# Kernel optimization log

Hardware: AMD Instinct MI355X
Metric: run time of the kernel (lower is better)

The kernel has to match this reference:

```python
import jax, jax.numpy as jnp
import numpy as np

N = 100000      # num nodes
E = 800000      # num edges
IN = 128        # in_channels
OUT = 128       # out_channels
ALPHA = 0.5


def setup_inputs() -> dict:
    key = jax.random.key(0)
    k1, k2, k3, k4, k5, k6 = jax.random.split(key, 6)
    x = jax.random.normal(k1, (N, IN), dtype=jnp.float32)
    edge_index = jax.random.randint(k2, (2, E), 0, N, dtype=jnp.int32)
    # GCNConv linear weights (glorot-ish) and biases for both directions
    s = 1.0 / np.sqrt(IN)
    W_sd = jax.random.normal(k3, (IN, OUT), dtype=jnp.float32) * s
    b_sd = jnp.zeros((OUT,), dtype=jnp.float32)
    W_ds = jax.random.normal(k4, (IN, OUT), dtype=jnp.float32) * s
    b_ds = jnp.zeros((OUT,), dtype=jnp.float32)
    return {"x": x, "edge_index": edge_index, "W_sd": W_sd, "b_sd": b_sd,
            "W_ds": W_ds, "b_ds": b_ds}


def _dir_gcn_norm_weights(row, col, dtype):
    """edge_weight = out_deg_inv_sqrt[row] * in_deg_inv_sqrt[col] (unit input weights)."""
    ones = jnp.ones((row.shape[0],), dtype=dtype)
    in_deg = jax.ops.segment_sum(ones, col, num_segments=N)
    out_deg = jax.ops.segment_sum(ones, row, num_segments=N)
    in_inv = jnp.where(in_deg > 0, jax.lax.rsqrt(in_deg), 0.0).astype(dtype)
    out_inv = jnp.where(out_deg > 0, jax.lax.rsqrt(out_deg), 0.0).astype(dtype)
    return out_inv[row] * in_inv[col]


def _gcn_conv(x, W, b, src, dst, w):
    """GCNConv(normalize=False, add_self_loops=False): lin -> gather -> scale -> scatter-add -> +bias."""
    h = x @ W                                   # [N, OUT]
    msg = h[src] * w[:, None]                   # [E, OUT]
    return jax.ops.segment_sum(msg, dst, num_segments=N) + b


def reference(x, edge_index, W_sd, b_sd, W_ds, b_ds):
    row, col = edge_index[0], edge_index[1]
    # forward-direction norm (src->dst) and transposed-graph norm (edge_index.flip(0))
    w = _dir_gcn_norm_weights(row, col, x.dtype)
    w_t = _dir_gcn_norm_weights(col, row, x.dtype)
    # conv_dst_to_src uses transposed edges: source=col, dest=row
    x_in = _gcn_conv(x, W_ds, b_ds, col, row, w_t)
    # conv_src_to_dst uses original edges: source=row, dest=col
    x_out = _gcn_conv(x, W_sd, b_sd, row, col, w)
    return ALPHA * x_in + (1.0 - ALPHA) * x_out
```

## Files before the change

kernel.cpp:

```cpp
#include <hip/hip_runtime.h>

#define NN 100000
#define NE 800000
#define NI 1600000
#define NB 391
#define IPB 6250

#define OFF_INV    0u
#define OFF_OFFS   800000u
#define OFF_BB     1600008u
#define OFF_HIST   1601600u
#define OFF_CSRC   2001984u
#define OFF_XB     8401984u
#define OFF_AGG    34001984u
#define OFF_PAIRS  34001984u
#define OFF_WT     85201984u
#define OFF_BIAS   85267520u
#define OFF_TOT    85268032u

typedef short short8 __attribute__((ext_vector_type(8)));
typedef unsigned short u16x8 __attribute__((ext_vector_type(8)));
typedef float f32x4 __attribute__((ext_vector_type(4)));
typedef float f32x8 __attribute__((ext_vector_type(8)));

__device__ __forceinline__ unsigned short f2bf(float f) {
    unsigned u = __float_as_uint(f);
    u = (u + 0x7FFFu + ((u >> 16) & 1u)) >> 16;
    return (unsigned short)u;
}
__device__ __forceinline__ float b2f(unsigned short h) {
    return __uint_as_float(((unsigned)h) << 16);
}
__device__ __forceinline__ f32x8 bvec2f(u16x8 v) {
    f32x8 r;
#pragma unroll
    for (int i = 0; i < 8; ++i) r[i] = b2f(v[i]);
    return r;
}


__global__ __launch_bounds__(256) void k_hist(const int* __restrict__ ei,
                                              int* __restrict__ hist) {
    __shared__ int h[NB];
    for (int k = threadIdx.x; k < NB; k += 256) h[k] = 0;
    __syncthreads();
    int base = blockIdx.x * IPB;
    for (int t = threadIdx.x; t < IPB; t += 256) {
        int i = base + t;
        int key = (i < NE) ? ei[i] : (NN + ei[i]);
        atomicAdd(&h[key >> 9], 1);
    }
    __syncthreads();
    for (int k = threadIdx.x; k < NB; k += 256) hist[k * 256 + blockIdx.x] = h[k];
}

__global__ __launch_bounds__(256) void k_red(const int* __restrict__ hist,
                                             int* __restrict__ tot) {
    __shared__ int s[256];
    int k = blockIdx.x;
    s[threadIdx.x] = hist[k * 256 + threadIdx.x];
    __syncthreads();
    for (int st = 128; st > 0; st >>= 1) {
        if (threadIdx.x < st) s[threadIdx.x] += s[threadIdx.x + st];
        __syncthreads();
    }
    if (threadIdx.x == 0) tot[k] = s[0];
}

__global__ __launch_bounds__(512) void k_scan_tot(const int* __restrict__ tot,
                                                  int* __restrict__ bb) {
    __shared__ int sA[512], sB[512];
    int tid = threadIdx.x;
    int v = (tid < NB) ? tot[tid] : 0;
    sA[tid] = v;
    __syncthreads();
    int *src = sA, *dst = sB;
    for (int st = 1; st < 512; st <<= 1) {
        dst[tid] = src[tid] + ((tid >= st) ? src[tid - st] : 0);
        __syncthreads();
        int* tp = src; src = dst; dst = tp;
    }
    if (tid <= NB) bb[tid] = (tid > 0) ? src[tid - 1] : 0;
}

__global__ __launch_bounds__(256) void k_rebase(int* __restrict__ hist,
                                                const int* __restrict__ bb) {
    __shared__ int sA[256], sB[256];
    int k = blockIdx.x, tid = threadIdx.x;
    int v = hist[k * 256 + tid];
    sA[tid] = v;
    __syncthreads();
    int *src = sA, *dst = sB;
    for (int st = 1; st < 256; st <<= 1) {
        dst[tid] = src[tid] + ((tid >= st) ? src[tid - st] : 0);
        __syncthreads();
        int* tp = src; src = dst; dst = tp;
    }
    hist[k * 256 + tid] = bb[k] + src[tid] - v;
}

__global__ __launch_bounds__(256) void k_scatter(const int* __restrict__ ei,
                                                 const int* __restrict__ hist,
                                                 unsigned long long* __restrict__ pairs) {
    __shared__ int cur[NB];
    for (int k = threadIdx.x; k < NB; k += 256) cur[k] = hist[k * 256 + blockIdx.x];
    __syncthreads();
    int base = blockIdx.x * IPB;
    for (int t = threadIdx.x; t < IPB; t += 256) {
        int i = base + t;
        int e = ei[i];
        int key, val;
        if (i < NE) { key = e;      val = ei[NE + i]; }
        else        { key = NN + e; val = ei[i - NE]; }
        int pos = atomicAdd(&cur[key >> 9], 1);
        pairs[pos] = (((unsigned long long)(unsigned)key) << 32) | (unsigned)val;
    }
}

__global__ __launch_bounds__(256) void k_bucket(const unsigned long long* __restrict__ pairs,
                                                const int* __restrict__ bb,
                                                int* __restrict__ csr_src,
                                                int* __restrict__ offsets,
                                                float* __restrict__ inv) {
    __shared__ int sA[512], sB[512], cur[512];
    const int h = blockIdx.x, tid = threadIdx.x;
    const int s0 = bb[h], s1 = bb[h + 1];
    for (int k = tid; k < 512; k += 256) sA[k] = 0;
    __syncthreads();
    for (int i = s0 + tid; i < s1; i += 256) {
        int key = (int)(pairs[i] >> 32);
        atomicAdd(&sA[key & 511], 1);
    }
    __syncthreads();
    int *src = sA, *dst = sB;
    for (int st = 1; st < 512; st <<= 1) {
        for (int k = tid; k < 512; k += 256) dst[k] = src[k] + ((k >= st) ? src[k - st] : 0);
        __syncthreads();
        int* tp = src; src = dst; dst = tp;
    }
    for (int k = tid; k < 512; k += 256) {
        int incl = src[k];
        int excl = (k > 0) ? src[k - 1] : 0;
        cur[k] = s0 + excl;
        int gkey = h * 512 + k;
        if (gkey <= 2 * NN) offsets[gkey] = s0 + excl;
        if (gkey < 2 * NN) {
            int cnt = incl - excl;
            inv[gkey] = (cnt > 0) ? rsqrtf((float)cnt) : 0.0f;
        }
    }
    __syncthreads();
    for (int i = s0 + tid; i < s1; i += 256) {
        unsigned long long p = pairs[i];
        int key = (int)(p >> 32);
        int pos = atomicAdd(&cur[key & 511], 1);
        csr_src[pos] = (int)(unsigned)(p & 0xffffffffULL);
    }
}

__global__ __launch_bounds__(256) void k_cvt_x(const float4* __restrict__ x4,
                                               ushort4* __restrict__ xb4) {
    int i = blockIdx.x * blockDim.x + threadIdx.x;
    if (i >= NN * 32) return;
    float4 v = x4[i];
    ushort4 o;
    o.x = f2bf(v.x); o.y = f2bf(v.y); o.z = f2bf(v.z); o.w = f2bf(v.w);
    xb4[i] = o;
}

__global__ void k_prep_w(const float* __restrict__ Wds, const float* __restrict__ Wsd,
                         const float* __restrict__ bds, const float* __restrict__ bsd,
                         unsigned short* __restrict__ wt, float* __restrict__ bias) {
    int id = blockIdx.x * blockDim.x + threadIdx.x;
    if (id >= 128 * 256) return;
    int c = id & 127;
    int k = id >> 7;
    float v = (k < 128) ? Wds[k * 128 + c] : Wsd[(k - 128) * 128 + c];
    wt[c * 256 + k] = f2bf(v);
    if (k == 0) bias[c] = 0.5f * (bds[c] + bsd[c]);
}

__global__ __launch_bounds__(256) void k_gather(
    const u16x8* __restrict__ xb8, const int* __restrict__ offsets,
    const int* __restrict__ csr_src, const float* __restrict__ inv,
    u16x8* __restrict__ agg8) {
    int wave = threadIdx.x >> 6;
    int lane = threadIdx.x & 63;
    int grp = lane >> 4;
    int cl = lane & 15;
    int n = blockIdx.x * 8 + wave * 2 + (grp >> 1);
    int dir = grp & 1;

    int key = dir * NN + n;
    int s0 = offsets[key], s1 = offsets[key + 1];
    const float* __restrict__ srcinv = inv + (dir ^ 1) * NN;

    f32x8 acc = {0.f, 0.f, 0.f, 0.f, 0.f, 0.f, 0.f, 0.f};
    int e = s0;
    for (; e + 4 <= s1; e += 4) {
        int i0 = csr_src[e];
        int i1 = csr_src[e + 1];
        int i2 = csr_src[e + 2];
        int i3 = csr_src[e + 3];
        float w0 = srcinv[i0], w1 = srcinv[i1], w2 = srcinv[i2], w3 = srcinv[i3];
        u16x8 v0 = xb8[i0 * 16 + cl];
        u16x8 v1 = xb8[i1 * 16 + cl];
        u16x8 v2 = xb8[i2 * 16 + cl];
        u16x8 v3 = xb8[i3 * 16 + cl];
        acc += w0 * bvec2f(v0);
        acc += w1 * bvec2f(v1);
        acc += w2 * bvec2f(v2);
        acc += w3 * bvec2f(v3);
    }
    for (; e < s1; ++e) {
        int i0 = csr_src[e];
        float w0 = srcinv[i0];
        u16x8 v0 = xb8[i0 * 16 + cl];
        acc += w0 * bvec2f(v0);
    }

    float ds = 0.5f * inv[dir * NN + n];
    u16x8 o;
#pragma unroll
    for (int i = 0; i < 8; ++i) o[i] = f2bf(acc[i] * ds);
    agg8[n * 32 + dir * 16 + cl] = o;
}

__global__ __launch_bounds__(256) void k_gemm_mfma(
    const unsigned short* __restrict__ agg, const unsigned short* __restrict__ wt,
    const float* __restrict__ bias, float* __restrict__ out) {
    const int wave = threadIdx.x >> 6;
    const int lane = threadIdx.x & 63;
    const int row0 = blockIdx.x * 64 + wave * 16;
    const int fr = lane & 15;
    const int kg = (lane >> 4) * 8;

    int arow = row0 + fr;
    if (arow >= NN) arow = 0;
    const unsigned short* aptr = agg + arow * 256 + kg;

    f32x4 acc[8] = {};

#pragma unroll
    for (int s = 0; s < 8; ++s) {
        short8 afrag = *(const short8*)(aptr + s * 32);
#pragma unroll
        for (int t = 0; t < 8; ++t) {
            short8 bfrag = *(const short8*)(wt + (t * 16 + fr) * 256 + s * 32 + kg);
            acc[t] = __builtin_amdgcn_mfma_f32_16x16x32_bf16(afrag, bfrag, acc[t], 0, 0, 0);
        }
    }

    const int orow0 = row0 + (lane >> 4) * 4;
#pragma unroll
    for (int i = 0; i < 4; ++i) {
        int orow = orow0 + i;
        if (orow < NN) {
#pragma unroll
            for (int t = 0; t < 8; ++t) {
                int col = t * 16 + fr;
                out[orow * 128 + col] = acc[t][i] + bias[col];
            }
        }
    }
}

extern "C" void kernel_launch(void* const* d_in, const int* in_sizes, int n_in,
                              void* d_out, int out_size, void* d_ws, size_t ws_size,
                              hipStream_t stream) {
    const float* x   = (const float*)d_in[0];
    const int* ei    = (const int*)d_in[1];
    const float* Wsd = (const float*)d_in[2];
    const float* bsd = (const float*)d_in[3];
    const float* Wds = (const float*)d_in[4];
    const float* bds = (const float*)d_in[5];

    char* ws = (char*)d_ws;
    float* inv     = (float*)(ws + OFF_INV);
    int*   offsets = (int*)(ws + OFF_OFFS);
    int*   bb      = (int*)(ws + OFF_BB);
    int*   hist    = (int*)(ws + OFF_HIST);
    int*   csr_src = (int*)(ws + OFF_CSRC);
    unsigned short* xb  = (unsigned short*)(ws + OFF_XB);
    unsigned short* agg = (unsigned short*)(ws + OFF_AGG);
    unsigned long long* pairs = (unsigned long long*)(ws + OFF_PAIRS);
    unsigned short* wt  = (unsigned short*)(ws + OFF_WT);
    float* bias    = (float*)(ws + OFF_BIAS);
    int*   tot     = (int*)(ws + OFF_TOT);

    k_cvt_x<<<(NN * 32 + 255) / 256, 256, 0, stream>>>((const float4*)x, (ushort4*)xb);
    k_prep_w<<<(128 * 256 + 255) / 256, 256, 0, stream>>>(Wds, Wsd, bds, bsd, wt, bias);
    k_hist<<<256, 256, 0, stream>>>(ei, hist);
    k_red<<<NB, 256, 0, stream>>>(hist, tot);
    k_scan_tot<<<1, 512, 0, stream>>>(tot, bb);
    k_rebase<<<NB, 256, 0, stream>>>(hist, bb);
    k_scatter<<<256, 256, 0, stream>>>(ei, hist, pairs);
    k_bucket<<<NB, 256, 0, stream>>>(pairs, bb, csr_src, offsets, inv);
    k_gather<<<NN / 8, 256, 0, stream>>>((const u16x8*)xb, offsets, csr_src, inv,
                                         (u16x8*)agg);
    k_gemm_mfma<<<(NN + 63) / 64, 256, 0, stream>>>(agg, wt, bias, (float*)d_out);
}
```

Before: 217.1 us.

## Fuse neighbor gather with MFMA GEMM via LDS and merge prep kernels

The gather now writes each block's 16 aggregated bf16 rows into shared memory, and the same block runs the MFMA GEMM on them. This removes the global agg buffer round trip and one kernel launch. The x conversion, weight prep and histogram kernels are merged into one launch that dispatches on block index. In exchange, every block reloads the transposed weights from cache and the GEMM tile shrinks to 16 rows.

```diff
diff --git a/kernel.cpp b/kernel.cpp
--- a/kernel.cpp
+++ b/kernel.cpp
@@ -5,6 +5,10 @@
 #define NI 1600000
 #define NB 391
 #define IPB 6250
+
+#define GB_CVT 12500
+#define GB_PW  128
+#define GB_HIST 256
 
 #define OFF_INV    0u
 #define OFF_OFFS   800000u
@@ -12,7 +16,6 @@
 #define OFF_HIST   1601600u
 #define OFF_CSRC   2001984u
 #define OFF_XB     8401984u
-#define OFF_AGG    34001984u
 #define OFF_PAIRS  34001984u
 #define OFF_WT     85201984u
 #define OFF_BIAS   85267520u
@@ -39,19 +42,42 @@
 }
 
 
-__global__ __launch_bounds__(256) void k_hist(const int* __restrict__ ei,
-                                              int* __restrict__ hist) {
+__global__ __launch_bounds__(256) void k_prep(
+    const float4* __restrict__ x4, ushort4* __restrict__ xb4,
+    const float* __restrict__ Wds, const float* __restrict__ Wsd,
+    const float* __restrict__ bds, const float* __restrict__ bsd,
+    unsigned short* __restrict__ wt, float* __restrict__ bias,
+    const int* __restrict__ ei, int* __restrict__ hist) {
     __shared__ int h[NB];
+    int bid = blockIdx.x;
+    if (bid < GB_CVT) {
+        int i = bid * 256 + threadIdx.x;
+        float4 v = x4[i];
+        ushort4 o;
+        o.x = f2bf(v.x); o.y = f2bf(v.y); o.z = f2bf(v.z); o.w = f2bf(v.w);
+        xb4[i] = o;
+        return;
+    }
+    if (bid < GB_CVT + GB_PW) {
+        int id = (bid - GB_CVT) * 256 + threadIdx.x;
+        int c = id & 127;
+        int k = id >> 7;
+        float v = (k < 128) ? Wds[k * 128 + c] : Wsd[(k - 128) * 128 + c];
+        wt[c * 256 + k] = f2bf(v);
+        if (k == 0) bias[c] = 0.5f * (bds[c] + bsd[c]);
+        return;
+    }
+    int hb = bid - GB_CVT - GB_PW;
     for (int k = threadIdx.x; k < NB; k += 256) h[k] = 0;
     __syncthreads();
-    int base = blockIdx.x * IPB;
+    int base = hb * IPB;
     for (int t = threadIdx.x; t < IPB; t += 256) {
         int i = base + t;
         int key = (i < NE) ? ei[i] : (NN + ei[i]);
         atomicAdd(&h[key >> 9], 1);
     }
     __syncthreads();
-    for (int k = threadIdx.x; k < NB; k += 256) hist[k * 256 + blockIdx.x] = h[k];
+    for (int k = threadIdx.x; k < NB; k += 256) hist[k * 256 + hb] = h[k];
 }
 
 __global__ __launch_bounds__(256) void k_red(const int* __restrict__ hist,
@@ -158,110 +184,75 @@
     }
 }
 
-__global__ __launch_bounds__(256) void k_cvt_x(const float4* __restrict__ x4,
-                                               ushort4* __restrict__ xb4) {
-    int i = blockIdx.x * blockDim.x + threadIdx.x;
-    if (i >= NN * 32) return;
-    float4 v = x4[i];
-    ushort4 o;
-    o.x = f2bf(v.x); o.y = f2bf(v.y); o.z = f2bf(v.z); o.w = f2bf(v.w);
-    xb4[i] = o;
-}
-
-__global__ void k_prep_w(const float* __restrict__ Wds, const float* __restrict__ Wsd,
-                         const float* __restrict__ bds, const float* __restrict__ bsd,
-                         unsigned short* __restrict__ wt, float* __restrict__ bias) {
-    int id = blockIdx.x * blockDim.x + threadIdx.x;
-    if (id >= 128 * 256) return;
-    int c = id & 127;
-    int k = id >> 7;
-    float v = (k < 128) ? Wds[k * 128 + c] : Wsd[(k - 128) * 128 + c];
-    wt[c * 256 + k] = f2bf(v);
-    if (k == 0) bias[c] = 0.5f * (bds[c] + bsd[c]);
-}
-
-__global__ __launch_bounds__(256) void k_gather(
+__global__ __launch_bounds__(512) void k_gather_gemm(
     const u16x8* __restrict__ xb8, const int* __restrict__ offsets,
     const int* __restrict__ csr_src, const float* __restrict__ inv,
-    u16x8* __restrict__ agg8) {
-    int wave = threadIdx.x >> 6;
-    int lane = threadIdx.x & 63;
-    int grp = lane >> 4;
-    int cl = lane & 15;
-    int n = blockIdx.x * 8 + wave * 2 + (grp >> 1);
-    int dir = grp & 1;
-
-    int key = dir * NN + n;
-    int s0 = offsets[key], s1 = offsets[key + 1];
-    const float* __restrict__ srcinv = inv + (dir ^ 1) * NN;
-
-    f32x8 acc = {0.f, 0.f, 0.f, 0.f, 0.f, 0.f, 0.f, 0.f};
-    int e = s0;
-    for (; e + 4 <= s1; e += 4) {
-        int i0 = csr_src[e];
-        int i1 = csr_src[e + 1];
-        int i2 = csr_src[e + 2];
-        int i3 = csr_src[e + 3];
-        float w0 = srcinv[i0], w1 = srcinv[i1], w2 = srcinv[i2], w3 = srcinv[i3];
-        u16x8 v0 = xb8[i0 * 16 + cl];
-        u16x8 v1 = xb8[i1 * 16 + cl];
-        u16x8 v2 = xb8[i2 * 16 + cl];
-        u16x8 v3 = xb8[i3 * 16 + cl];
-        acc += w0 * bvec2f(v0);
-        acc += w1 * bvec2f(v1);
-        acc += w2 * bvec2f(v2);
-        acc += w3 * bvec2f(v3);
-    }
-    for (; e < s1; ++e) {
-        int i0 = csr_src[e];
-        float w0 = srcinv[i0];
-        u16x8 v0 = xb8[i0 * 16 + cl];
-        acc += w0 * bvec2f(v0);
-    }
-
-    float ds = 0.5f * inv[dir * NN + n];
-    u16x8 o;
-#pragma unroll
-    for (int i = 0; i < 8; ++i) o[i] = f2bf(acc[i] * ds);
-    agg8[n * 32 + dir * 16 + cl] = o;
-}
-
-__global__ __launch_bounds__(256) void k_gemm_mfma(
-    const unsigned short* __restrict__ agg, const unsigned short* __restrict__ wt,
-    const float* __restrict__ bias, float* __restrict__ out) {
+    const unsigned short* __restrict__ wt, const float* __restrict__ bias,
+    float* __restrict__ out) {
+    __shared__ unsigned short a_lds[16][264];
+
     const int wave = threadIdx.x >> 6;
     const int lane = threadIdx.x & 63;
-    const int row0 = blockIdx.x * 64 + wave * 16;
+    const int grp = lane >> 4;
+    const int cl = lane & 15;
+    const int nl = wave * 2 + (grp >> 1);
+    const int n = blockIdx.x * 16 + nl;
+    const int dir = grp & 1;
+
+    {
+        int key = dir * NN + n;
+        int s0 = offsets[key], s1 = offsets[key + 1];
+        const float* __restrict__ srcinv = inv + (dir ^ 1) * NN;
+
+        f32x8 acc = {0.f, 0.f, 0.f, 0.f, 0.f, 0.f, 0.f, 0.f};
+        int e = s0;
+        for (; e + 4 <= s1; e += 4) {
+            int i0 = csr_src[e];
+            int i1 = csr_src[e + 1];
+            int i2 = csr_src[e + 2];
+            int i3 = csr_src[e + 3];
+            float w0 = srcinv[i0], w1 = srcinv[i1], w2 = srcinv[i2], w3 = srcinv[i3];
+            u16x8 v0 = xb8[i0 * 16 + cl];
+            u16x8 v1 = xb8[i1 * 16 + cl];
+            u16x8 v2 = xb8[i2 * 16 + cl];
+            u16x8 v3 = xb8[i3 * 16 + cl];
+            acc += w0 * bvec2f(v0);
+            acc += w1 * bvec2f(v1);
+            acc += w2 * bvec2f(v2);
+            acc += w3 * bvec2f(v3);
+        }
+        for (; e < s1; ++e) {
+            int i0 = csr_src[e];
+            float w0 = srcinv[i0];
+            u16x8 v0 = xb8[i0 * 16 + cl];
+            acc += w0 * bvec2f(v0);
+        }
+
+        float ds = 0.5f * inv[dir * NN + n];
+        u16x8 o;
+#pragma unroll
+        for (int i = 0; i < 8; ++i) o[i] = f2bf(acc[i] * ds);
+        *(u16x8*)&a_lds[nl][dir * 128 + cl * 8] = o;
+    }
+    __syncthreads();
+
     const int fr = lane & 15;
     const int kg = (lane >> 4) * 8;
-
-    int arow = row0 + fr;
-    if (arow >= NN) arow = 0;
-    const unsigned short* aptr = agg + arow * 256 + kg;
-
-    f32x4 acc[8] = {};
-
+    const int col = wave * 16 + fr;
+
+    f32x4 acc = {};
 #pragma unroll
     for (int s = 0; s < 8; ++s) {
-        short8 afrag = *(const short8*)(aptr + s * 32);
-#pragma unroll
-        for (int t = 0; t < 8; ++t) {
-            short8 bfrag = *(const short8*)(wt + (t * 16 + fr) * 256 + s * 32 + kg);
-            acc[t] = __builtin_amdgcn_mfma_f32_16x16x32_bf16(afrag, bfrag, acc[t], 0, 0, 0);
-        }
-    }
-
-    const int orow0 = row0 + (lane >> 4) * 4;
+        short8 afrag = *(const short8*)&a_lds[fr][s * 32 + kg];
+        short8 bfrag = *(const short8*)(wt + col * 256 + s * 32 + kg);
+        acc = __builtin_amdgcn_mfma_f32_16x16x32_bf16(afrag, bfrag, acc, 0, 0, 0);
+    }
+
+    const float b = bias[col];
+    const int orow0 = blockIdx.x * 16 + (lane >> 4) * 4;
 #pragma unroll
     for (int i = 0; i < 4; ++i) {
-        int orow = orow0 + i;
-        if (orow < NN) {
-#pragma unroll
-            for (int t = 0; t < 8; ++t) {
-                int col = t * 16 + fr;
-                out[orow * 128 + col] = acc[t][i] + bias[col];
-            }
-        }
+        out[(orow0 + i) * 128 + col] = acc[i] + b;
     }
 }
 
@@ -282,21 +273,18 @@
     int*   hist    = (int*)(ws + OFF_HIST);
     int*   csr_src = (int*)(ws + OFF_CSRC);
     unsigned short* xb  = (unsigned short*)(ws + OFF_XB);
-    unsigned short* agg = (unsigned short*)(ws + OFF_AGG);
     unsigned long long* pairs = (unsigned long long*)(ws + OFF_PAIRS);
     unsigned short* wt  = (unsigned short*)(ws + OFF_WT);
     float* bias    = (float*)(ws + OFF_BIAS);
     int*   tot     = (int*)(ws + OFF_TOT);
 
-    k_cvt_x<<<(NN * 32 + 255) / 256, 256, 0, stream>>>((const float4*)x, (ushort4*)xb);
-    k_prep_w<<<(128 * 256 + 255) / 256, 256, 0, stream>>>(Wds, Wsd, bds, bsd, wt, bias);
-    k_hist<<<256, 256, 0, stream>>>(ei, hist);
+    k_prep<<<GB_CVT + GB_PW + GB_HIST, 256, 0, stream>>>(
+        (const float4*)x, (ushort4*)xb, Wds, Wsd, bds, bsd, wt, bias, ei, hist);
     k_red<<<NB, 256, 0, stream>>>(hist, tot);
     k_scan_tot<<<1, 512, 0, stream>>>(tot, bb);
     k_rebase<<<NB, 256, 0, stream>>>(hist, bb);
     k_scatter<<<256, 256, 0, stream>>>(ei, hist, pairs);
     k_bucket<<<NB, 256, 0, stream>>>(pairs, bb, csr_src, offsets, inv);
-    k_gather<<<NN / 8, 256, 0, stream>>>((const u16x8*)xb, offsets, csr_src, inv,
-                                         (u16x8*)agg);
-    k_gemm_mfma<<<(NN + 63) / 64, 256, 0, stream>>>(agg, wt, bias, (float*)d_out);
-}
+    k_gather_gemm<<<NN / 16, 512, 0, stream>>>((const u16x8*)xb, offsets, csr_src, inv,
+                                               wt, bias, (float*)d_out);
+}
```

New measurement: 179.5 us. -17.3%, faster.
